# Performance work log

Measured on AMD Instinct MI355X. Metric: run time of the kernel, lower is better.

## Reference

```python
import jax, jax.numpy as jnp
import numpy as np

RESOLUTION = 1_000_000  # number of candidate phase patterns in the lookup table
N_ANTS = 32             # antennas / feature dim summed over


def setup_inputs() -> dict:
    key = jax.random.key(0)
    k1, k2 = jax.random.split(key)
    two_pi = 2.0 * np.pi
    # Codebook of possible phase patterns, [resolution, n_ants], phases in [0, 2*pi)
    possible_phases = jax.random.uniform(k1, (RESOLUTION, N_ANTS), dtype=jnp.float32) * two_pi
    phases = jax.random.uniform(k2, (N_ANTS,), dtype=jnp.float32) * two_pi
    return {"possible_phases": possible_phases, "phases": phases}


def reference(possible_phases, phases):
    # similarity[r] = sum_a (possible_phases[r, a] - phases[a])^2 ; return global min
    diff = possible_phases - phases  # [R, A] broadcast over rows
    similarity = jnp.sum(diff * diff, axis=1)  # [R]
    return jnp.min(similarity)  # scalar
```

## Files before the change

### kernel.cpp

```cpp
#include <hip/hip_runtime.h>


__global__ __launch_bounds__(256) void doa_stage_kernel(
    const float* __restrict__ pp,
    const float* __restrict__ ph,
    float* __restrict__ ws,
    int R)
{
    __shared__ float4 lds[256 * 9];

    const int t = threadIdx.x;
    const long long base_row = (long long)blockIdx.x * 256;

    float q[32];
#pragma unroll
    for (int a = 0; a < 32; ++a) q[a] = ph[a];

    const float4* src = reinterpret_cast<const float4*>(pp);
    const long long gmax = (long long)R * 8;
    float4 v[8];
#pragma unroll
    for (int i = 0; i < 8; ++i) {
        long long g = base_row * 8 + i * 256 + t;
        if (g >= gmax) g = 0;
        v[i] = src[g];
    }
#pragma unroll
    for (int i = 0; i < 8; ++i) {
        const int idx = i * 256 + t;
        lds[(idx >> 3) * 9 + (idx & 7)] = v[i];
    }
    __syncthreads();

    float s = __builtin_inff();
    if (base_row + t < R) {
        s = 0.0f;
#pragma unroll
        for (int k = 0; k < 8; ++k) {
            const float4 p = lds[t * 9 + k];
            const float dx = p.x - q[4 * k + 0];
            const float dy = p.y - q[4 * k + 1];
            const float dz = p.z - q[4 * k + 2];
            const float dw = p.w - q[4 * k + 3];
            s += dx * dx + dy * dy + dz * dz + dw * dw;
        }
    }

#pragma unroll
    for (int off = 1; off < 64; off <<= 1)
        s = fminf(s, __shfl_xor(s, off));

    __shared__ float wmin[4];
    const int lane = t & 63;
    const int wid  = t >> 6;
    if (lane == 0) wmin[wid] = s;
    __syncthreads();
    if (t == 0) {
        ws[blockIdx.x] = fminf(fminf(wmin[0], wmin[1]), fminf(wmin[2], wmin[3]));
    }
}

__global__ __launch_bounds__(1024) void doa_reduce_kernel(
    const float* __restrict__ ws,
    float* __restrict__ out,
    int n)
{
    float s = __builtin_inff();
    for (int i = threadIdx.x; i < n; i += 1024)
        s = fminf(s, ws[i]);

#pragma unroll
    for (int off = 1; off < 64; off <<= 1)
        s = fminf(s, __shfl_xor(s, off));

    __shared__ float wmin[16];
    if ((threadIdx.x & 63) == 0) wmin[threadIdx.x >> 6] = s;
    __syncthreads();
    if (threadIdx.x == 0) {
        float m = wmin[0];
#pragma unroll
        for (int w = 1; w < 16; ++w) m = fminf(m, wmin[w]);
        *out = m;
    }
}

extern "C" void kernel_launch(void* const* d_in, const int* in_sizes, int n_in,
                              void* d_out, int out_size, void* d_ws, size_t ws_size,
                              hipStream_t stream) {
    const float* pp = (const float*)d_in[0];
    const float* ph = (const float*)d_in[1];
    float* out = (float*)d_out;
    float* ws  = (float*)d_ws;

    const int R = in_sizes[0] / 32;
    const int grid = (R + 255) / 256;

    doa_stage_kernel<<<grid, 256, 0, stream>>>(pp, ph, ws, R);
    doa_reduce_kernel<<<1, 1024, 0, stream>>>(ws, out, grid);
}
```

Before: 26.45 us.

## Replace LDS transpose with 8-lane shuffle reduction; vectorize final min-reduce loads

New measurement: 25.60 us (median of 2 runs). 3.2% less time.

```diff
diff --git a/kernel.cpp b/kernel.cpp
--- a/kernel.cpp
+++ b/kernel.cpp
@@ -7,14 +7,10 @@
     float* __restrict__ ws,
     int R)
 {
-    __shared__ float4 lds[256 * 9];
-
     const int t = threadIdx.x;
     const long long base_row = (long long)blockIdx.x * 256;
 
-    float q[32];
-#pragma unroll
-    for (int a = 0; a < 32; ++a) q[a] = ph[a];
+    const float4 qk = reinterpret_cast<const float4*>(ph)[t & 7];
 
     const float4* src = reinterpret_cast<const float4*>(pp);
     const long long gmax = (long long)R * 8;
@@ -25,35 +21,28 @@
         if (g >= gmax) g = 0;
         v[i] = src[g];
     }
+
+    float lmin = __builtin_inff();
 #pragma unroll
     for (int i = 0; i < 8; ++i) {
-        const int idx = i * 256 + t;
-        lds[(idx >> 3) * 9 + (idx & 7)] = v[i];
-    }
-    __syncthreads();
-
-    float s = __builtin_inff();
-    if (base_row + t < R) {
-        s = 0.0f;
-#pragma unroll
-        for (int k = 0; k < 8; ++k) {
-            const float4 p = lds[t * 9 + k];
-            const float dx = p.x - q[4 * k + 0];
-            const float dy = p.y - q[4 * k + 1];
-            const float dz = p.z - q[4 * k + 2];
-            const float dw = p.w - q[4 * k + 3];
-            s += dx * dx + dy * dy + dz * dz + dw * dw;
-        }
+        const float dx = v[i].x - qk.x;
+        const float dy = v[i].y - qk.y;
+        const float dz = v[i].z - qk.z;
+        const float dw = v[i].w - qk.w;
+        float s = dx * dx + dy * dy + dz * dz + dw * dw;
+        s += __shfl_xor(s, 1);
+        s += __shfl_xor(s, 2);
+        s += __shfl_xor(s, 4);
+        const long long row = base_row + i * 32 + (t >> 3);
+        if (row < R) lmin = fminf(lmin, s);
     }
 
-#pragma unroll
-    for (int off = 1; off < 64; off <<= 1)
-        s = fminf(s, __shfl_xor(s, off));
+    lmin = fminf(lmin, __shfl_xor(lmin, 8));
+    lmin = fminf(lmin, __shfl_xor(lmin, 16));
+    lmin = fminf(lmin, __shfl_xor(lmin, 32));
 
     __shared__ float wmin[4];
-    const int lane = t & 63;
-    const int wid  = t >> 6;
-    if (lane == 0) wmin[wid] = s;
+    if ((t & 63) == 0) wmin[t >> 6] = lmin;
     __syncthreads();
     if (t == 0) {
         ws[blockIdx.x] = fminf(fminf(wmin[0], wmin[1]), fminf(wmin[2], wmin[3]));
@@ -65,18 +54,24 @@
     float* __restrict__ out,
     int n)
 {
+    const int t = threadIdx.x;
+    const int n4 = n >> 2;
+
     float s = __builtin_inff();
-    for (int i = threadIdx.x; i < n; i += 1024)
-        s = fminf(s, ws[i]);
+    for (int i = t; i < n4; i += 1024) {
+        const float4 p = reinterpret_cast<const float4*>(ws)[i];
+        s = fminf(fminf(s, fminf(p.x, p.y)), fminf(p.z, p.w));
+    }
+    if (t < (n & 3)) s = fminf(s, ws[(n4 << 2) + t]);
 
 #pragma unroll
     for (int off = 1; off < 64; off <<= 1)
         s = fminf(s, __shfl_xor(s, off));
 
     __shared__ float wmin[16];
-    if ((threadIdx.x & 63) == 0) wmin[threadIdx.x >> 6] = s;
+    if ((t & 63) == 0) wmin[t >> 6] = s;
     __syncthreads();
-    if (threadIdx.x == 0) {
+    if (t == 0) {
         float m = wmin[0];
 #pragma unroll
         for (int w = 1; w < 16; ++w) m = fminf(m, wmin[w]);
```
